# Kernel optimization log

Measured on AMD Instinct MI355X. Metric: run time of the kernel, lower is better.

Reference implementation:

```python
import jax, jax.numpy as jnp
import numpy as np

N = 100000      # nodes
E = 1600000     # edges
IN_DIM = 256
H = 128         # hidden_mlp == hidden_gnn
Z = 32          # latent_dim
HD = 128        # hidden_dec


def _lin(k, fan_in, fan_out):
    # torch nn.Linear default init: U(-1/sqrt(fan_in), 1/sqrt(fan_in))
    kw, kb = jax.random.split(k)
    lim = 1.0 / np.sqrt(fan_in)
    W = jax.random.uniform(kw, (fan_in, fan_out), jnp.float32, -lim, lim)
    b = jax.random.uniform(kb, (fan_out,), jnp.float32, -lim, lim)
    return W, b


def setup_inputs() -> dict:
    key = jax.random.key(0)
    ks = jax.random.split(key, 16)
    x = jax.random.normal(ks[0], (N, IN_DIM), jnp.float32)
    edge_index = jax.random.randint(ks[1], (2, E), 0, N, jnp.int64)
    edge_attr = jax.random.uniform(ks[2], (E,), jnp.float32)

    W1, b1 = _lin(ks[3], IN_DIM, H)       # encoder mlp layer 1
    W2, b2 = _lin(ks[4], H, H)            # encoder mlp layer 2
    Wrel1, brel1 = _lin(ks[5], H, H)      # gnn1 lin_rel
    Wroot1, _ = _lin(ks[6], H, H)         # gnn1 lin_root (no bias)
    Wrel2, brel2 = _lin(ks[7], H, H)      # gnn2 lin_rel
    Wroot2, _ = _lin(ks[8], H, H)         # gnn2 lin_root
    Wmu, bmu = _lin(ks[9], H, Z)
    Wlv, blv = _lin(ks[10], H, Z)
    Wd1, bd1 = _lin(ks[11], Z, HD)
    Wd2, bd2 = _lin(ks[12], HD, IN_DIM)
    eps = jax.random.normal(ks[13], (N, Z), jnp.float32)  # reparam noise (fixed)

    return dict(x=x, edge_index=edge_index, edge_attr=edge_attr,
                W1=W1, b1=b1, W2=W2, b2=b2,
                Wrel1=Wrel1, brel1=brel1, Wroot1=Wroot1,
                Wrel2=Wrel2, brel2=brel2, Wroot2=Wroot2,
                Wmu=Wmu, bmu=bmu, Wlv=Wlv, blv=blv,
                Wd1=Wd1, bd1=bd1, Wd2=Wd2, bd2=bd2, eps=eps)


def _graph_conv(h, src, dst, w, Wrel, brel, Wroot):
    # PyG GraphConv (aggr='add'): out_i = lin_rel(sum_{j->i} w_ji * h_j) + lin_root(h_i)
    msgs = h[src] * w[:, None]                       # [E, H] gather
    agg = jax.ops.segment_sum(msgs, dst, num_segments=N)  # [N, H] scatter-add
    return agg @ Wrel + brel + h @ Wroot


def reference(x, edge_index, edge_attr,
              W1, b1, W2, b2,
              Wrel1, brel1, Wroot1,
              Wrel2, brel2, Wroot2,
              Wmu, bmu, Wlv, blv,
              Wd1, bd1, Wd2, bd2, eps):
    src, dst = edge_index[0], edge_index[1]
    # encoder MLP
    h = jax.nn.relu(x @ W1 + b1)
    h = jax.nn.relu(h @ W2 + b2)
    # two GraphConv message-passing layers with ReLU
    h = jax.nn.relu(_graph_conv(h, src, dst, edge_attr, Wrel1, brel1, Wroot1))
    h = jax.nn.relu(_graph_conv(h, src, dst, edge_attr, Wrel2, brel2, Wroot2))
    # heads
    mu = h @ Wmu + bmu
    logvar = h @ Wlv + blv
    # reparameterize with fixed eps
    z = mu + eps * jnp.exp(0.5 * logvar)
    # decoder MLP
    x_recon = jax.nn.relu(z @ Wd1 + bd1) @ Wd2 + bd2
    return x_recon, mu, logvar, z
```

## Files before the change

### kernel.cpp

```cpp
#include <hip/hip_runtime.h>
#include <math.h>

#define NN 100000
#define EE 1600000
#define NB 1563

typedef _Float16 f16;
typedef __attribute__((ext_vector_type(2))) _Float16 f16x2;
typedef __attribute__((ext_vector_type(8))) _Float16 f16x8;
typedef __attribute__((ext_vector_type(4))) float f32x4;
typedef unsigned int u32;

__device__ __forceinline__ float frelu(float v){ return v > 0.f ? v : 0.f; }

__device__ __forceinline__ f32x4 mfma16(f16x8 a, f16x8 b, f32x4 c){
    return __builtin_amdgcn_mfma_f32_16x16x32_f16(a, b, c, 0, 0, 0);
}

__device__ __forceinline__ int2 nt_load_int2(const int2* p){
    long long v = __builtin_nontemporal_load((const long long*)p);
    int2 r; r.x = (int)(v & 0xFFFFFFFFll); r.y = (int)(v >> 32);
    return r;
}

__global__ __launch_bounds__(256) void hist_pack(const int* __restrict__ dst,
                                                 int* __restrict__ totals,
                                                 int* __restrict__ blockhist,
                                                 const float* __restrict__ W1,
                                                 const float* __restrict__ W2,
                                                 const float* __restrict__ Wrel1,
                                                 const float* __restrict__ Wroot1,
                                                 const float* __restrict__ Wrel2,
                                                 const float* __restrict__ Wroot2,
                                                 const float* __restrict__ Wd1,
                                                 const float* __restrict__ Wd2,
                                                 const float* __restrict__ Wmu,
                                                 const float* __restrict__ Wlv,
                                                 f16* __restrict__ pack)
{
    __shared__ int cntS[NB];
    const int t = threadIdx.x;
    if (blockIdx.x < 250) {
        const int blk = blockIdx.x;
        for (int i = t; i < NB; i += 256) cntS[i] = 0;
        __syncthreads();
        const int ebase = blk * 6400;
        #pragma unroll
        for (int i = 0; i < 25; i++) {
            int k = dst[ebase + i * 256 + t] >> 6;
            atomicAdd(&cntS[k], 1);
        }
        __syncthreads();
        for (int i = t; i < NB; i += 256) {
            int c = cntS[i];
            blockhist[blk * NB + i] = c;
            if (c) atomicAdd(&totals[i], c);
        }
        return;
    }
    int tt = (blockIdx.x - 250) * 256 + t;
    float v;
    if (tt < 32768) {
        int l = tt;
        int j = l & 7, lane = (l >> 3) & 63, ct = (l >> 9) & 7, kk = l >> 12;
        int k = kk * 32 + ((lane >> 4) << 3) + j, c = (ct << 4) + (lane & 15);
        v = W1[k * 128 + c];
    } else if (tt < 49152) {
        int l = tt - 32768;
        int j = l & 7, lane = (l >> 3) & 63, ct = (l >> 9) & 7, kk = l >> 12;
        int k = kk * 32 + ((lane >> 4) << 3) + j, c = (ct << 4) + (lane & 15);
        v = W2[k * 128 + c];
    } else if (tt < 81920) {
        int l = tt - 49152;
        int j = l & 7, lane = (l >> 3) & 63, ct = (l >> 9) & 7, kk = l >> 12;
        int k = kk * 32 + ((lane >> 4) << 3) + j, c = (ct << 4) + (lane & 15);
        v = (k < 128) ? Wrel1[k * 128 + c] : Wroot1[(k - 128) * 128 + c];
    } else if (tt < 114688) {
        int l = tt - 81920;
        int j = l & 7, lane = (l >> 3) & 63, ct = (l >> 9) & 7, kk = l >> 12;
        int k = kk * 32 + ((lane >> 4) << 3) + j, c = (ct << 4) + (lane & 15);
        v = (k < 128) ? Wrel2[k * 128 + c] : Wroot2[(k - 128) * 128 + c];
    } else if (tt < 118784) {
        int l = tt - 114688;
        int j = l & 7, lane = (l >> 3) & 63, ct = (l >> 9) & 7;
        int k = ((lane >> 4) << 3) + j, c = (ct << 4) + (lane & 15);
        v = Wd1[k * 128 + c];
    } else if (tt < 151552) {
        int l = tt - 118784;
        int j = l & 7, lane = (l >> 3) & 63, ct = (l >> 9) & 15, kk = l >> 13;
        int k = kk * 32 + ((lane >> 4) << 3) + j, c = (ct << 4) + (lane & 15);
        v = Wd2[k * 256 + c];
    } else {
        int l = tt - 151552;
        int j = l & 7, lane = (l >> 3) & 63, ct = (l >> 9) & 3, kk = l >> 11;
        int k = kk * 32 + ((lane >> 4) << 3) + j, c = (ct << 4) + (lane & 15);
        v = (c < 32) ? Wmu[k * 32 + c] : Wlv[k * 32 + (c - 32)];
    }
    pack[tt] = (f16)v;
}

__global__ __launch_bounds__(256) void colscan(int* __restrict__ blockhist)
{
    __shared__ int lds[256];
    const int t = threadIdx.x, k = blockIdx.x;
    int v = (t < 250) ? blockhist[t * NB + k] : 0;
    lds[t] = v;
    __syncthreads();
    for (int off = 1; off < 256; off <<= 1) {
        int y = (t >= off) ? lds[t - off] : 0;
        __syncthreads();
        lds[t] += y;
        __syncthreads();
    }
    if (t < 250) blockhist[t * NB + k] = lds[t] - v;
}

__global__ __launch_bounds__(256) void scatter(const int* __restrict__ src,
                                               const int* __restrict__ dst,
                                               const float* __restrict__ ea,
                                               const int* __restrict__ totals,
                                               const int* __restrict__ blockhist,
                                               int* __restrict__ bs_g,
                                               int2* __restrict__ tmp)
{
    __shared__ int bsS[NB + 1];
    __shared__ int tmpS[256];
    __shared__ int carryS;
    __shared__ int prefS[NB];
    __shared__ int cntS[NB];
    const int t = threadIdx.x, blk = blockIdx.x;
    if (t == 0) carryS = 0;
    __syncthreads();
    for (int c = 0; c < 7; c++) {
        int idx = c * 256 + t;
        int val = (idx < NB) ? totals[idx] : 0;
        tmpS[t] = val;
        __syncthreads();
        for (int off = 1; off < 256; off <<= 1) {
            int y = (t >= off) ? tmpS[t - off] : 0;
            __syncthreads();
            tmpS[t] += y;
            __syncthreads();
        }
        if (idx < NB) bsS[idx] = carryS + tmpS[t] - val;
        __syncthreads();
        if (t == 255) carryS += tmpS[255];
        __syncthreads();
    }
    if (t == 0) bsS[NB] = carryS;
    for (int i = t; i < NB; i += 256) {
        prefS[i] = blockhist[blk * NB + i];
        cntS[i] = 0;
    }
    __syncthreads();
    if (blk == 0)
        for (int i = t; i < NB + 1; i += 256) bs_g[i] = bsS[i];
    const int ebase = blk * 6400;
    #pragma unroll
    for (int i = 0; i < 25; i++) {
        int e = ebase + i * 256 + t;
        int d = dst[e];
        int k = d >> 6;
        int rank = atomicAdd(&cntS[k], 1);
        int pos = bsS[k] + prefS[k] + rank;
        tmp[pos] = make_int2(src[e] | ((d & 63) << 17), __float_as_int(ea[e]));
    }
}

__global__ __launch_bounds__(256) void bucket_sort(const int2* __restrict__ tmp,
                                                   const int* __restrict__ bs_g,
                                                   int2* __restrict__ pairs,
                                                   int* __restrict__ offsets,
                                                   int* __restrict__ counts)
{
    __shared__ int hist[64], excl[64], cursor[64];
    const int t = threadIdx.x, k = blockIdx.x;
    const int start = bs_g[k], end = bs_g[k + 1];
    if (t < 64) hist[t] = 0;
    __syncthreads();
    for (int i = start + t; i < end; i += 256)
        atomicAdd(&hist[(tmp[i].x >> 17) & 63], 1);
    __syncthreads();
    if (t == 0) {
        int run = 0;
        #pragma unroll
        for (int j = 0; j < 64; j++) { excl[j] = run; cursor[j] = run; run += hist[j]; }
    }
    __syncthreads();
    for (int i = start + t; i < end; i += 256) {
        int2 e = tmp[i];
        int local = (e.x >> 17) & 63;
        int rank = atomicAdd(&cursor[local], 1);
        pairs[start + rank] = make_int2(e.x & 0x1FFFF, e.y);
    }
    if (t < 64) {
        int node = (k << 6) + t;
        if (node < NN) {
            counts[node]  = hist[t];
            offsets[node] = start + excl[t] + hist[t];
        }
    }
}

__global__ __launch_bounds__(256) void agg_q(const f16* __restrict__ h,
                                             const int2* __restrict__ pairs,
                                             const int* __restrict__ offsets,
                                             const int* __restrict__ counts,
                                             f16* __restrict__ out)
{
    const int gt   = blockIdx.x * 256 + threadIdx.x;
    const int node = gt >> 4;
    const int ch   = gt & 15;
    const int end  = offsets[node];
    int i = end - counts[node];
    float acc[8];
    #pragma unroll
    for (int j = 0; j < 8; j++) acc[j] = 0.f;
    const uint4* __restrict__ h16 = (const uint4*)h;
    for (; i + 2 <= end; i += 2) {
        int2 p0 = nt_load_int2(pairs + i);
        int2 p1 = nt_load_int2(pairs + i + 1);
        uint4 r0 = h16[(size_t)p0.x * 16 + ch];
        uint4 r1 = h16[(size_t)p1.x * 16 + ch];
        float w0 = __int_as_float(p0.y), w1 = __int_as_float(p1.y);
        const f16* e0 = (const f16*)&r0;
        const f16* e1 = (const f16*)&r1;
        #pragma unroll
        for (int j = 0; j < 8; j++) acc[j] = fmaf(w0, (float)e0[j], acc[j]);
        #pragma unroll
        for (int j = 0; j < 8; j++) acc[j] = fmaf(w1, (float)e1[j], acc[j]);
    }
    if (i < end) {
        int2 p0 = nt_load_int2(pairs + i);
        uint4 r0 = h16[(size_t)p0.x * 16 + ch];
        float w0 = __int_as_float(p0.y);
        const f16* e0 = (const f16*)&r0;
        #pragma unroll
        for (int j = 0; j < 8; j++) acc[j] = fmaf(w0, (float)e0[j], acc[j]);
    }
    union { f16 hh[8]; uint4 u; } cv;
    #pragma unroll
    for (int j = 0; j < 8; j++) cv.hh[j] = (f16)acc[j];
    ((uint4*)out)[(size_t)node * 16 + ch] = cv.u;
}

template<int C>
__device__ __forceinline__ void stage_tile(const float* __restrict__ src, int nbase,
                                           f16* lds, int ldr, int colofs)
{
    const int t = threadIdx.x;
    #pragma unroll
    for (int i = 0; i < (64 * C / 4) / 256; i++) {
        int elem = t + i * 256;
        int row = elem / (C / 4);
        int c4  = elem % (C / 4);
        int srow = nbase + row; if (srow >= NN) srow = NN - 1;
        float4 v = *(const float4*)(src + (size_t)srow * C + c4 * 4);
        union { f16 h[4]; uint2 u; } cv;
        cv.h[0] = (f16)v.x; cv.h[1] = (f16)v.y; cv.h[2] = (f16)v.z; cv.h[3] = (f16)v.w;
        *(uint2*)&lds[row * ldr + colofs + c4 * 4] = cv.u;
    }
}

template<int C>
__device__ __forceinline__ void stage_tile_f16(const f16* __restrict__ src, int nbase,
                                               f16* lds, int ldr, int colofs)
{
    const int t = threadIdx.x;
    #pragma unroll
    for (int i = 0; i < (64 * C / 4) / 256; i++) {
        int elem = t + i * 256;
        int row = elem / (C / 4);
        int c4  = elem % (C / 4);
        int srow = nbase + row; if (srow >= NN) srow = NN - 1;
        uint2 v = *(const uint2*)(src + (size_t)srow * C + c4 * 4);
        *(uint2*)&lds[row * ldr + colofs + c4 * 4] = v;
    }
}

template<int K, int CT>
__device__ __forceinline__ void wave_gemm(const f16* lds, int ldr,
                                          const f16x8* __restrict__ wp, f32x4 acc[CT])
{
    const int lane = threadIdx.x & 63;
    const int wrow = (threadIdx.x >> 6) * 16;
    const int arow = wrow + (lane & 15);
    const int kofs = (lane >> 4) << 3;
    #pragma unroll
    for (int kk = 0; kk < K / 32; kk++) {
        f16x8 a = *(const f16x8*)&lds[arow * ldr + kk * 32 + kofs];
        #pragma unroll
        for (int ct = 0; ct < CT; ct++) {
            f16x8 b = wp[(kk * CT + ct) * 64 + lane];
            acc[ct] = mfma16(a, b, acc[ct]);
        }
    }
}

template<int CT>
__device__ __forceinline__ void zacc(f32x4 acc[CT])
{
    #pragma unroll
    for (int ct = 0; ct < CT; ct++) acc[ct] = f32x4{0.f, 0.f, 0.f, 0.f};
}

template<int CT, bool RELU>
__device__ __forceinline__ void store_f32(float* __restrict__ dst, int OUTC, int nbase,
                                          const float* __restrict__ bias, f32x4 acc[CT])
{
    const int lane = threadIdx.x & 63;
    const int wrow = (threadIdx.x >> 6) * 16;
    #pragma unroll
    for (int ct = 0; ct < CT; ct++) {
        int c = ct * 16 + (lane & 15);
        float bv = bias[c];
        #pragma unroll
        for (int r = 0; r < 4; r++) {
            int node = nbase + wrow + ((lane >> 4) << 2) + r;
            if (node < NN) {
                float v = acc[ct][r] + bv;
                if (RELU) v = frelu(v);
                dst[(size_t)node * OUTC + c] = v;
            }
        }
    }
}

template<int CT, bool RELU>
__device__ __forceinline__ void store_f16g(f16* __restrict__ dst, int OUTC, int nbase,
                                           const float* __restrict__ bias, f32x4 acc[CT])
{
    const int lane = threadIdx.x & 63;
    const int wrow = (threadIdx.x >> 6) * 16;
    #pragma unroll
    for (int ct = 0; ct < CT; ct++) {
        int c = ct * 16 + (lane & 15);
        float bv = bias[c];
        #pragma unroll
        for (int r = 0; r < 4; r++) {
            int node = nbase + wrow + ((lane >> 4) << 2) + r;
            if (node < NN) {
                float v = acc[ct][r] + bv;
                if (RELU) v = frelu(v);
                dst[(size_t)node * OUTC + c] = (f16)v;
            }
        }
    }
}

template<int CT>
__device__ __forceinline__ void store_lds_f16(f16* lds, int ldr,
                                              const float* __restrict__ bias, f32x4 acc[CT])
{
    const int lane = threadIdx.x & 63;
    const int wrow = (threadIdx.x >> 6) * 16;
    #pragma unroll
    for (int ct = 0; ct < CT; ct++) {
        int c = ct * 16 + (lane & 15);
        float bv = bias[c];
        #pragma unroll
        for (int r = 0; r < 4; r++) {
            int row = wrow + ((lane >> 4) << 2) + r;
            lds[row * ldr + c] = (f16)frelu(acc[ct][r] + bv);
        }
    }
}

__global__ __launch_bounds__(256) void enc_mfma(const float* __restrict__ x,
                                                const f16x8* __restrict__ wp1,
                                                const f16x8* __restrict__ wp2,
                                                const float* __restrict__ b1,
                                                const float* __restrict__ b2,
                                                f16* __restrict__ out)
{
    __shared__ __align__(16) f16 xs[64 * 264];
    __shared__ __align__(16) f16 h1[64 * 136];
    const int nbase = blockIdx.x * 64;
    stage_tile<256>(x, nbase, xs, 264, 0);
    __syncthreads();
    f32x4 acc[8];
    zacc<8>(acc);
    wave_gemm<256, 8>(xs, 264, wp1, acc);
    store_lds_f16<8>(h1, 136, b1, acc);
    __syncthreads();
    zacc<8>(acc);
    wave_gemm<128, 8>(h1, 136, wp2, acc);
    store_f16g<8, true>(out, 128, nbase, b2, acc);
}

__global__ __launch_bounds__(256) void conv_mfma(const f16* __restrict__ agg,
                                                 const f16* __restrict__ h,
                                                 const f16x8* __restrict__ wp,
                                                 const float* __restrict__ brel,
                                                 f16* __restrict__ out)
{
    __shared__ __align__(16) f16 as_[64 * 264];
    const int nbase = blockIdx.x * 64;
    stage_tile_f16<128>(agg, nbase, as_, 264, 0);
    stage_tile_f16<128>(h,   nbase, as_, 264, 128);
    __syncthreads();
    f32x4 acc[8];
    zacc<8>(acc);
    wave_gemm<256, 8>(as_, 264, wp, acc);
    store_f16g<8, true>(out, 128, nbase, brel, acc);
}

__global__ __launch_bounds__(256) void heads_mfma(const f16* __restrict__ h,
                                                  const f16x8* __restrict__ wp,
                                                  const float* __restrict__ bmu,
                                                  const float* __restrict__ blv,
                                                  const float* __restrict__ eps,
                                                  float* __restrict__ out)
{
    __shared__ __align__(16) f16 hs[64 * 136];
    __shared__ __align__(16) float muS[64 * 32];
    __shared__ __align__(16) float lvS[64 * 32];
    const int nbase = blockIdx.x * 64;
    stage_tile_f16<128>(h, nbase, hs, 136, 0);
    __syncthreads();
    f32x4 acc[4];
    zacc<4>(acc);
    wave_gemm<128, 4>(hs, 136, wp, acc);
    const int lane = threadIdx.x & 63;
    const int wrow = (threadIdx.x >> 6) * 16;
    #pragma unroll
    for (int ct = 0; ct < 4; ct++) {
        int c = ct * 16 + (lane & 15);
        bool ismu = (c < 32);
        int cc = c & 31;
        float bv = ismu ? bmu[cc] : blv[cc];
        float* gbase = out + (ismu ? (size_t)25600000 : (size_t)28800000);
        float* sb = ismu ? muS : lvS;
        #pragma unroll
        for (int r = 0; r < 4; r++) {
            int row = wrow + ((lane >> 4) << 2) + r;
            int node = nbase + row;
            float v = acc[ct][r] + bv;
            sb[row * 32 + cc] = v;
            if (node < NN) gbase[(size_t)node * 32 + cc] = v;
        }
    }
    __syncthreads();
    {
        const int node = threadIdx.x >> 2;
        const int ch0  = (threadIdx.x & 3) * 8;
        const int gn = nbase + node;
        if (gn < NN) {
            const size_t g = (size_t)gn * 32 + ch0;
            float4 e0 = *(const float4*)(eps + g);
            float4 e1 = *(const float4*)(eps + g + 4);
            const float* mu = &muS[node * 32 + ch0];
            const float* lv = &lvS[node * 32 + ch0];
            float4 z0, z1;
            z0.x = fmaf(e0.x, expf(0.5f * lv[0]), mu[0]);
            z0.y = fmaf(e0.y, expf(0.5f * lv[1]), mu[1]);
            z0.z = fmaf(e0.z, expf(0.5f * lv[2]), mu[2]);
            z0.w = fmaf(e0.w, expf(0.5f * lv[3]), mu[3]);
            z1.x = fmaf(e1.x, expf(0.5f * lv[4]), mu[4]);
            z1.y = fmaf(e1.y, expf(0.5f * lv[5]), mu[5]);
            z1.z = fmaf(e1.z, expf(0.5f * lv[6]), mu[6]);
            z1.w = fmaf(e1.w, expf(0.5f * lv[7]), mu[7]);
            *(float4*)(out + 32000000 + g) = z0;
            *(float4*)(out + 32000000 + g + 4) = z1;
        }
    }
}

__global__ __launch_bounds__(256) void dec_mfma(const float* __restrict__ z,
                                                const f16x8* __restrict__ wp1,
                                                const float* __restrict__ bd1,
                                                const f16x8* __restrict__ wp2,
                                                const float* __restrict__ bd2,
                                                float* __restrict__ out)
{
    __shared__ __align__(16) f16 zs[64 * 40];
    __shared__ __align__(16) f16 hd[64 * 136];
    const int nbase = blockIdx.x * 64;
    stage_tile<32>(z, nbase, zs, 40, 0);
    __syncthreads();
    f32x4 acc[8];
    zacc<8>(acc);
    wave_gemm<32, 8>(zs, 40, wp1, acc);
    store_lds_f16<8>(hd, 136, bd1, acc);
    __syncthreads();
    f32x4 acc2[16];
    zacc<16>(acc2);
    wave_gemm<128, 16>(hd, 136, wp2, acc2);
    store_f32<16, false>(out, 256, nbase, bd2, acc2);
}

extern "C" void kernel_launch(void* const* d_in, const int* in_sizes, int n_in,
                              void* d_out, int out_size, void* d_ws, size_t ws_size,
                              hipStream_t stream)
{
    const float* x     = (const float*)d_in[0];
    const int*   ei    = (const int*)d_in[1];
    const float* ea    = (const float*)d_in[2];
    const float* W1    = (const float*)d_in[3];
    const float* b1    = (const float*)d_in[4];
    const float* W2    = (const float*)d_in[5];
    const float* b2    = (const float*)d_in[6];
    const float* Wrel1 = (const float*)d_in[7];
    const float* brel1 = (const float*)d_in[8];
    const float* Wroot1= (const float*)d_in[9];
    const float* Wrel2 = (const float*)d_in[10];
    const float* brel2 = (const float*)d_in[11];
    const float* Wroot2= (const float*)d_in[12];
    const float* Wmu   = (const float*)d_in[13];
    const float* bmu   = (const float*)d_in[14];
    const float* Wlv   = (const float*)d_in[15];
    const float* blv   = (const float*)d_in[16];
    const float* Wd1   = (const float*)d_in[17];
    const float* bd1   = (const float*)d_in[18];
    const float* Wd2   = (const float*)d_in[19];
    const float* bd2   = (const float*)d_in[20];
    const float* eps   = (const float*)d_in[21];
    float* out = (float*)d_out;

    f16* B0 = (f16*)out;
    f16* B1 = B0 + 12800000;

    char* ws = (char*)d_ws;
    int*  totals    = (int*) (ws);
    int*  blockhist = (int*) (ws + 8192);
    int*  bs_g      = (int*) (ws + 1571200);
    int2* tmp       = (int2*)(ws + 1577472);
    int2* pairs     = (int2*)(ws + 14377472);
    int*  offsets   = (int*) (ws + 27177472);
    int*  counts    = (int*) (ws + 27577472);
    f16*  pack      = (f16*) (ws + 27977472);

    const f16x8* wp_enc1  = (const f16x8*)(pack);
    const f16x8* wp_enc2  = (const f16x8*)(pack + 32768);
    const f16x8* wp_conv1 = (const f16x8*)(pack + 49152);
    const f16x8* wp_conv2 = (const f16x8*)(pack + 81920);
    const f16x8* wp_dec1  = (const f16x8*)(pack + 114688);
    const f16x8* wp_dec2  = (const f16x8*)(pack + 118784);
    const f16x8* wp_heads = (const f16x8*)(pack + 151552);

    const int* src = ei;
    const int* dst = ei + EE;

    hipMemsetAsync(totals, 0, 8192, stream);
    hist_pack<<<874, 256, 0, stream>>>(dst, totals, blockhist, W1, W2, Wrel1,
                                       Wroot1, Wrel2, Wroot2, Wd1, Wd2, Wmu, Wlv, pack);
    colscan<<<NB, 256, 0, stream>>>(blockhist);
    scatter<<<250, 256, 0, stream>>>(src, dst, ea, totals, blockhist, bs_g, tmp);
    bucket_sort<<<NB, 256, 0, stream>>>(tmp, bs_g, pairs, offsets, counts);

    enc_mfma<<<1563, 256, 0, stream>>>(x, wp_enc1, wp_enc2, b1, b2, B0);
    agg_q<<<6250, 256, 0, stream>>>(B0, pairs, offsets, counts, B1);
    conv_mfma<<<1563, 256, 0, stream>>>(B1, B0, wp_conv1, brel1, B1);
    agg_q<<<6250, 256, 0, stream>>>(B1, pairs, offsets, counts, B0);
    conv_mfma<<<1563, 256, 0, stream>>>(B0, B1, wp_conv2, brel2, B0);
    heads_mfma<<<1563, 256, 0, stream>>>(B0, wp_heads, bmu, blv, eps, out);
    dec_mfma<<<1563, 256, 0, stream>>>(out + 32000000, wp_dec1, bd1, wp_dec2, bd2, out);
}
```

Baseline: 426.8 us.

## Fuse conv2, heads and decoder into one tail kernel; compute totals in colscan

Merges the second GraphConv GEMM, the mu/logvar heads with reparameterization, and the two-layer decoder into one per-tile kernel. The intermediate activations stay in LDS instead of round-tripping through global memory, and z is no longer reread from global. Bucket totals now come from the column scan, which drops the global atomics and the memset. Intermediate buffers move from the output region into the workspace. The fused kernel uses more LDS per block, which may lower occupancy.

```diff
diff --git a/kernel.cpp b/kernel.cpp
--- a/kernel.cpp
+++ b/kernel.cpp
@@ -24,7 +24,6 @@
 }
 
 __global__ __launch_bounds__(256) void hist_pack(const int* __restrict__ dst,
-                                                 int* __restrict__ totals,
                                                  int* __restrict__ blockhist,
                                                  const float* __restrict__ W1,
                                                  const float* __restrict__ W2,
@@ -51,11 +50,8 @@
             atomicAdd(&cntS[k], 1);
         }
         __syncthreads();
-        for (int i = t; i < NB; i += 256) {
-            int c = cntS[i];
-            blockhist[blk * NB + i] = c;
-            if (c) atomicAdd(&totals[i], c);
-        }
+        for (int i = t; i < NB; i += 256)
+            blockhist[blk * NB + i] = cntS[i];
         return;
     }
     int tt = (blockIdx.x - 250) * 256 + t;
@@ -99,7 +95,8 @@
     pack[tt] = (f16)v;
 }
 
-__global__ __launch_bounds__(256) void colscan(int* __restrict__ blockhist)
+__global__ __launch_bounds__(256) void colscan(int* __restrict__ blockhist,
+                                               int* __restrict__ totals)
 {
     __shared__ int lds[256];
     const int t = threadIdx.x, k = blockIdx.x;
@@ -113,6 +110,7 @@
         __syncthreads();
     }
     if (t < 250) blockhist[t * NB + k] = lds[t] - v;
+    if (t == 255) totals[k] = lds[255];
 }
 
 __global__ __launch_bounds__(256) void scatter(const int* __restrict__ src,
@@ -405,24 +403,43 @@
     store_f16g<8, true>(out, 128, nbase, brel, acc);
 }
 
-__global__ __launch_bounds__(256) void heads_mfma(const f16* __restrict__ h,
-                                                  const f16x8* __restrict__ wp,
-                                                  const float* __restrict__ bmu,
-                                                  const float* __restrict__ blv,
-                                                  const float* __restrict__ eps,
-                                                  float* __restrict__ out)
-{
-    __shared__ __align__(16) f16 hs[64 * 136];
+__global__ __launch_bounds__(256) void tail_mfma(const f16* __restrict__ agg,
+                                                 const f16* __restrict__ h,
+                                                 const f16x8* __restrict__ wp_c2,
+                                                 const float* __restrict__ brel2,
+                                                 const f16x8* __restrict__ wp_hd,
+                                                 const float* __restrict__ bmu,
+                                                 const float* __restrict__ blv,
+                                                 const f16x8* __restrict__ wp_d1,
+                                                 const float* __restrict__ bd1,
+                                                 const f16x8* __restrict__ wp_d2,
+                                                 const float* __restrict__ bd2,
+                                                 const float* __restrict__ eps,
+                                                 float* __restrict__ out)
+{
+    __shared__ __align__(16) f16 as_[64 * 264];
+    __shared__ __align__(16) f16 hd[64 * 136];
+    __shared__ __align__(16) f16 zf[64 * 40];
     __shared__ __align__(16) float muS[64 * 32];
     __shared__ __align__(16) float lvS[64 * 32];
     const int nbase = blockIdx.x * 64;
-    stage_tile_f16<128>(h, nbase, hs, 136, 0);
-    __syncthreads();
-    f32x4 acc[4];
-    zacc<4>(acc);
-    wave_gemm<128, 4>(hs, 136, wp, acc);
-    const int lane = threadIdx.x & 63;
-    const int wrow = (threadIdx.x >> 6) * 16;
+    const int t = threadIdx.x;
+    const int lane = t & 63;
+    const int wrow = (t >> 6) * 16;
+
+    stage_tile_f16<128>(agg, nbase, as_, 264, 0);
+    stage_tile_f16<128>(h,   nbase, as_, 264, 128);
+    __syncthreads();
+    f32x4 acc8[8];
+    zacc<8>(acc8);
+    wave_gemm<256, 8>(as_, 264, wp_c2, acc8);
+    __syncthreads();
+    store_lds_f16<8>(as_, 136, brel2, acc8);
+    __syncthreads();
+
+    f32x4 acc4[4];
+    zacc<4>(acc4);
+    wave_gemm<128, 4>(as_, 136, wp_hd, acc4);
     #pragma unroll
     for (int ct = 0; ct < 4; ct++) {
         int c = ct * 16 + (lane & 15);
@@ -435,58 +452,53 @@
         for (int r = 0; r < 4; r++) {
             int row = wrow + ((lane >> 4) << 2) + r;
             int node = nbase + row;
-            float v = acc[ct][r] + bv;
+            float v = acc4[ct][r] + bv;
             sb[row * 32 + cc] = v;
             if (node < NN) gbase[(size_t)node * 32 + cc] = v;
         }
     }
     __syncthreads();
+
     {
-        const int node = threadIdx.x >> 2;
-        const int ch0  = (threadIdx.x & 3) * 8;
+        const int node = t >> 2;
+        const int ch0  = (t & 3) * 8;
         const int gn = nbase + node;
+        const float* mu = &muS[node * 32 + ch0];
+        const float* lv = &lvS[node * 32 + ch0];
+        float4 e0 = make_float4(0.f, 0.f, 0.f, 0.f), e1 = e0;
         if (gn < NN) {
             const size_t g = (size_t)gn * 32 + ch0;
-            float4 e0 = *(const float4*)(eps + g);
-            float4 e1 = *(const float4*)(eps + g + 4);
-            const float* mu = &muS[node * 32 + ch0];
-            const float* lv = &lvS[node * 32 + ch0];
-            float4 z0, z1;
-            z0.x = fmaf(e0.x, expf(0.5f * lv[0]), mu[0]);
-            z0.y = fmaf(e0.y, expf(0.5f * lv[1]), mu[1]);
-            z0.z = fmaf(e0.z, expf(0.5f * lv[2]), mu[2]);
-            z0.w = fmaf(e0.w, expf(0.5f * lv[3]), mu[3]);
-            z1.x = fmaf(e1.x, expf(0.5f * lv[4]), mu[4]);
-            z1.y = fmaf(e1.y, expf(0.5f * lv[5]), mu[5]);
-            z1.z = fmaf(e1.z, expf(0.5f * lv[6]), mu[6]);
-            z1.w = fmaf(e1.w, expf(0.5f * lv[7]), mu[7]);
-            *(float4*)(out + 32000000 + g) = z0;
-            *(float4*)(out + 32000000 + g + 4) = z1;
-        }
-    }
-}
-
-__global__ __launch_bounds__(256) void dec_mfma(const float* __restrict__ z,
-                                                const f16x8* __restrict__ wp1,
-                                                const float* __restrict__ bd1,
-                                                const f16x8* __restrict__ wp2,
-                                                const float* __restrict__ bd2,
-                                                float* __restrict__ out)
-{
-    __shared__ __align__(16) f16 zs[64 * 40];
-    __shared__ __align__(16) f16 hd[64 * 136];
-    const int nbase = blockIdx.x * 64;
-    stage_tile<32>(z, nbase, zs, 40, 0);
-    __syncthreads();
-    f32x4 acc[8];
-    zacc<8>(acc);
-    wave_gemm<32, 8>(zs, 40, wp1, acc);
-    store_lds_f16<8>(hd, 136, bd1, acc);
-    __syncthreads();
-    f32x4 acc2[16];
-    zacc<16>(acc2);
-    wave_gemm<128, 16>(hd, 136, wp2, acc2);
-    store_f32<16, false>(out, 256, nbase, bd2, acc2);
+            e0 = *(const float4*)(eps + g);
+            e1 = *(const float4*)(eps + g + 4);
+        }
+        float zv[8];
+        zv[0] = fmaf(e0.x, expf(0.5f * lv[0]), mu[0]);
+        zv[1] = fmaf(e0.y, expf(0.5f * lv[1]), mu[1]);
+        zv[2] = fmaf(e0.z, expf(0.5f * lv[2]), mu[2]);
+        zv[3] = fmaf(e0.w, expf(0.5f * lv[3]), mu[3]);
+        zv[4] = fmaf(e1.x, expf(0.5f * lv[4]), mu[4]);
+        zv[5] = fmaf(e1.y, expf(0.5f * lv[5]), mu[5]);
+        zv[6] = fmaf(e1.z, expf(0.5f * lv[6]), mu[6]);
+        zv[7] = fmaf(e1.w, expf(0.5f * lv[7]), mu[7]);
+        if (gn < NN) {
+            const size_t g = (size_t)gn * 32 + ch0;
+            *(float4*)(out + 32000000 + g)     = make_float4(zv[0], zv[1], zv[2], zv[3]);
+            *(float4*)(out + 32000000 + g + 4) = make_float4(zv[4], zv[5], zv[6], zv[7]);
+        }
+        #pragma unroll
+        for (int j = 0; j < 8; j++) zf[node * 40 + ch0 + j] = (f16)zv[j];
+    }
+    __syncthreads();
+
+    f32x4 accd[8];
+    zacc<8>(accd);
+    wave_gemm<32, 8>(zf, 40, wp_d1, accd);
+    store_lds_f16<8>(hd, 136, bd1, accd);
+    __syncthreads();
+    f32x4 acc16[16];
+    zacc<16>(acc16);
+    wave_gemm<128, 16>(hd, 136, wp_d2, acc16);
+    store_f32<16, false>(out, 256, nbase, bd2, acc16);
 }
 
 extern "C" void kernel_launch(void* const* d_in, const int* in_sizes, int n_in,
@@ -517,9 +529,6 @@
     const float* eps   = (const float*)d_in[21];
     float* out = (float*)d_out;
 
-    f16* B0 = (f16*)out;
-    f16* B1 = B0 + 12800000;
-
     char* ws = (char*)d_ws;
     int*  totals    = (int*) (ws);
     int*  blockhist = (int*) (ws + 8192);
@@ -529,6 +538,8 @@
     int*  offsets   = (int*) (ws + 27177472);
     int*  counts    = (int*) (ws + 27577472);
     f16*  pack      = (f16*) (ws + 27977472);
+    f16*  B0        = (f16*) (ws + 28300000);
+    f16*  B1        = (f16*) (ws + 53900000);
 
     const f16x8* wp_enc1  = (const f16x8*)(pack);
     const f16x8* wp_enc2  = (const f16x8*)(pack + 32768);
@@ -541,10 +552,9 @@
     const int* src = ei;
     const int* dst = ei + EE;
 
-    hipMemsetAsync(totals, 0, 8192, stream);
-    hist_pack<<<874, 256, 0, stream>>>(dst, totals, blockhist, W1, W2, Wrel1,
-                                       Wroot1, Wrel2, Wroot2, Wd1, Wd2, Wmu, Wlv, pack);
-    colscan<<<NB, 256, 0, stream>>>(blockhist);
+    hist_pack<<<874, 256, 0, stream>>>(dst, blockhist, W1, W2, Wrel1, Wroot1,
+                                       Wrel2, Wroot2, Wd1, Wd2, Wmu, Wlv, pack);
+    colscan<<<NB, 256, 0, stream>>>(blockhist, totals);
     scatter<<<250, 256, 0, stream>>>(src, dst, ea, totals, blockhist, bs_g, tmp);
     bucket_sort<<<NB, 256, 0, stream>>>(tmp, bs_g, pairs, offsets, counts);
 
@@ -552,7 +562,6 @@
     agg_q<<<6250, 256, 0, stream>>>(B0, pairs, offsets, counts, B1);
     conv_mfma<<<1563, 256, 0, stream>>>(B1, B0, wp_conv1, brel1, B1);
     agg_q<<<6250, 256, 0, stream>>>(B1, pairs, offsets, counts, B0);
-    conv_mfma<<<1563, 256, 0, stream>>>(B0, B1, wp_conv2, brel2, B0);
-    heads_mfma<<<1563, 256, 0, stream>>>(B0, wp_heads, bmu, blv, eps, out);
-    dec_mfma<<<1563, 256, 0, stream>>>(out + 32000000, wp_dec1, bd1, wp_dec2, bd2, out);
-}
+    tail_mfma<<<1563, 256, 0, stream>>>(B0, B1, wp_conv2, brel2, wp_heads, bmu, blv,
+                                        wp_dec1, bd1, wp_dec2, bd2, eps, out);
+}
```

Result: slower. 465.8 us (+9.1%).
